# Kernel tuning notes

Measured on AMD Instinct MI355X. Metric: run time of the kernel, lower is better.

The kernel has to match this reference:

```python
import jax, jax.numpy as jnp
import numpy as np

NUM_HEADS = 16
EPS = 1e-5


def setup_inputs() -> dict:
    key = jax.random.key(0)
    ks = jax.random.split(key, 9)
    B, S, D = 2, 2048, 1024
    s = 1.0 / np.sqrt(D)
    return {
        "x": jax.random.normal(ks[0], (B, S, D), dtype=jnp.float32),
        "Wq": jax.random.uniform(ks[1], (D, D), jnp.float32, -s, s),
        "bq": jax.random.uniform(ks[2], (D,), jnp.float32, -s, s),
        "Wk": jax.random.uniform(ks[3], (D, D), jnp.float32, -s, s),
        "bk": jax.random.uniform(ks[4], (D,), jnp.float32, -s, s),
        "Wv": jax.random.uniform(ks[5], (D, D), jnp.float32, -s, s),
        "bv": jax.random.uniform(ks[6], (D,), jnp.float32, -s, s),
        "Wo": jax.random.uniform(ks[7], (D, D), jnp.float32, -s, s),
        "bo": jax.random.uniform(ks[8], (D,), jnp.float32, -s, s),
    }


def reference(x, Wq, bq, Wk, bk, Wv, bv, Wo, bo):
    B, S, D = x.shape
    H = NUM_HEADS
    hd = D // H
    # projections -> [B, H, S, hd]
    def proj(W, b):
        return (x @ W + b).reshape(B, S, H, hd).transpose(0, 2, 1, 3)
    Q = proj(Wq, bq)
    K = proj(Wk, bk)
    V = proj(Wv, bv)
    scores = jnp.einsum("bhqd,bhkd->bhqk", Q, K) / jnp.sqrt(jnp.float32(hd))
    attn = jax.nn.softmax(scores, axis=-1)  # dropout is identity in eval mode
    out = jnp.einsum("bhqk,bhkd->bhqd", attn, V)
    out = out.transpose(0, 2, 1, 3).reshape(B, S, D)
    out = jax.nn.relu(out @ Wo + bo)
    mu = jnp.mean(out, axis=-1, keepdims=True)
    var = jnp.var(out, axis=-1, keepdims=True)
    return (out - mu) * jax.lax.rsqrt(var + EPS)
```

## Files before the change

kernel.cpp:

```cpp
#include <hip/hip_runtime.h>
#include <hip/hip_bf16.h>
#include <math.h>

#define Bb 2
#define Ss 2048
#define Dd 1024
#define Hh 16
#define HD 64
#define Mm (Bb*Ss)

typedef __attribute__((ext_vector_type(8))) short bf8_t;
typedef __attribute__((ext_vector_type(4))) float f4_t;
typedef __attribute__((ext_vector_type(4))) unsigned u4_t;
typedef __attribute__((ext_vector_type(2))) unsigned uint2v;

#define LOG2E 1.4426950408889634f

#define AS1 __attribute__((address_space(1)))
#define AS3 __attribute__((address_space(3)))

__device__ __forceinline__ void gl2lds16(const void* g, void* l) {
    __builtin_amdgcn_global_load_lds((const AS1 unsigned int*)g,
                                     (AS3 unsigned int*)l, 16, 0, 0);
}
__device__ __forceinline__ short bfr(float f) {
    __hip_bfloat16 h = __float2bfloat16(f);
    return *reinterpret_cast<short*>(&h);
}
__device__ __forceinline__ unsigned pkbf16(float a, float b) {
    const unsigned ua = __builtin_bit_cast(unsigned, a) + 0x8000u;
    const unsigned ub = __builtin_bit_cast(unsigned, b) + 0x8000u;
    return __builtin_amdgcn_perm(ub, ua, 0x07060302u);
}
__device__ __forceinline__ float fexp2(float x) {
    return __builtin_amdgcn_exp2f(x);
}
__device__ __forceinline__ float b2f(unsigned short u) {
    return __builtin_bit_cast(float, (unsigned)u << 16);
}
__device__ __forceinline__ void pl32(unsigned &a, unsigned &b) {
#if __has_builtin(__builtin_amdgcn_permlane32_swap)
    uint2v r = __builtin_amdgcn_permlane32_swap(a, b, false, false);
    a = r[0]; b = r[1];
#else
    asm volatile("v_permlane32_swap_b32 %0, %1" : "+v"(a), "+v"(b));
#endif
}
__device__ __forceinline__ void pl16(unsigned &a, unsigned &b) {
#if __has_builtin(__builtin_amdgcn_permlane16_swap)
    uint2v r = __builtin_amdgcn_permlane16_swap(a, b, false, false);
    a = r[0]; b = r[1];
#else
    asm volatile("v_permlane16_swap_b32 %0, %1" : "+v"(a), "+v"(b));
#endif
}

__global__ __launch_bounds__(256)
void prep(const float* __restrict__ x,
          const float* __restrict__ w0, const float* __restrict__ w1,
          const float* __restrict__ w2, const float* __restrict__ w3,
          __hip_bfloat16* __restrict__ Wt4, __hip_bfloat16* __restrict__ Xh)
{
    const int z = blockIdx.z;
    if (z < 4) {
        const float* W = (z == 0) ? w0 : (z == 1) ? w1 : (z == 2) ? w2 : w3;
        __hip_bfloat16* Wt = Wt4 + (size_t)z * Dd * Dd;
        __shared__ float t[32][33];
        const int n0 = blockIdx.x * 32, k0 = blockIdx.y * 32;
        const int tx = threadIdx.x & 31, ty = threadIdx.x >> 5;
        #pragma unroll
        for (int rr = 0; rr < 4; ++rr)
            t[ty + rr*8][tx] = W[(size_t)(k0 + ty + rr*8) * Dd + n0 + tx];
        __syncthreads();
        #pragma unroll
        for (int rr = 0; rr < 4; ++rr)
            Wt[(size_t)(n0 + ty + rr*8) * Dd + k0 + tx] =
                __float2bfloat16(t[tx][ty + rr*8]);
    } else {
        const int bid = (z - 4) * 1024 + blockIdx.y * 32 + blockIdx.x;
        const size_t i = ((size_t)bid * 256 + threadIdx.x) * 8;
        const float4 a = *(const float4*)&x[i];
        const float4 b = *(const float4*)&x[i + 4];
        bf8_t o;
        o[0] = bfr(a.x); o[1] = bfr(a.y); o[2] = bfr(a.z); o[3] = bfr(a.w);
        o[4] = bfr(b.x); o[5] = bfr(b.y); o[6] = bfr(b.z); o[7] = bfr(b.w);
        *(bf8_t*)&Xh[i] = o;
    }
}

__global__ __launch_bounds__(256)
void gemm_qkv(const __hip_bfloat16* __restrict__ A,
              const __hip_bfloat16* __restrict__ Bt,
              const float* __restrict__ b0, const float* __restrict__ b1,
              const float* __restrict__ b2,
              __hip_bfloat16* __restrict__ Qh, __hip_bfloat16* __restrict__ Kh,
              __hip_bfloat16* __restrict__ Vt)
{
    __shared__ __align__(16) char pool[34816];
    __hip_bfloat16* As = (__hip_bfloat16*)pool;
    __hip_bfloat16* Bs = As + 2 * 128 * 32;

    const int lin  = blockIdx.y * 24 + blockIdx.x;
    const int nlin = (lin & 7) * 96 + (lin >> 3);
    const int bx   = nlin % 24;
    const int by   = nlin / 24;

    const int tid  = threadIdx.x;
    const int wave = tid >> 6;
    const int lane = tid & 63;
    const int llo  = lane & 15;
    const int lhi  = lane >> 4;
    const int wm   = wave & 1;
    const int wn   = wave >> 1;
    const int row0 = by * 128;
    const int col0 = bx * 128;

    size_t aoff[2], boff[2];
    int    loff[2];
    #pragma unroll
    for (int p = 0; p < 2; ++p) {
        const int g = p * 256 + wave * 64 + lane;
        const int r = g >> 2;
        const int kc = ((g & 3) ^ ((r >> 1) & 3)) * 8;
        aoff[p] = (size_t)(row0 + r) * Dd + kc;
        boff[p] = (size_t)(col0 + r) * Dd + kc;
        loff[p] = (p * 256 + wave * 64) * 16;
    }
    const __hip_bfloat16* Acur = A;
    const __hip_bfloat16* Bcur = Bt;

    auto stage = [&](int buf) {
        #pragma unroll
        for (int p = 0; p < 2; ++p) {
            gl2lds16(Acur + aoff[p], (char*)As + buf*8192 + loff[p]);
            gl2lds16(Bcur + boff[p], (char*)Bs + buf*8192 + loff[p]);
        }
        Acur += 32; Bcur += 32;
    };

    const int xch = (lhi ^ ((llo >> 1) & 3)) * 8;

    f4_t acc[4][4] = {};
    stage(0);
    for (int kt = 0; kt < 32; ++kt) {
        const int buf = kt & 1;
        __syncthreads();
        if (kt + 1 < 32) stage(buf ^ 1);

        bf8_t a[4], b[4];
        #pragma unroll
        for (int i = 0; i < 4; ++i)
            a[i] = *(const bf8_t*)&As[buf*4096 + (wm*64 + i*16 + llo) * 32 + xch];
        #pragma unroll
        for (int j = 0; j < 4; ++j)
            b[j] = *(const bf8_t*)&Bs[buf*4096 + (wn*64 + j*16 + llo) * 32 + xch];
        #pragma unroll
        for (int i = 0; i < 4; ++i)
            #pragma unroll
            for (int j = 0; j < 4; ++j)
                acc[i][j] = __builtin_amdgcn_mfma_f32_16x16x32_bf16(
                    a[i], b[j], acc[i][j], 0, 0, 0);
    }

    const int sel   = col0 >> 10;
    const int cbase = col0 & 1023;
    __hip_bfloat16* Ls = (__hip_bfloat16*)pool;
    __syncthreads();

    float bv[4];
    const float* bp = (sel == 0) ? b0 : (sel == 1) ? b1 : b2;
    #pragma unroll
    for (int j = 0; j < 4; ++j) bv[j] = bp[cbase + wn*64 + j*16 + llo];
    const float scale = (sel == 0) ? 0.125f * LOG2E : 1.0f;

    if (sel < 2) {
        #pragma unroll
        for (int i = 0; i < 4; ++i)
            #pragma unroll
            for (int r = 0; r < 4; ++r) {
                const int ml = wm*64 + i*16 + lhi*4 + r;
                #pragma unroll
                for (int j = 0; j < 4; ++j)
                    Ls[ml*136 + wn*64 + j*16 + llo] =
                        __float2bfloat16((acc[i][j][r] + bv[j]) * scale);
            }
        __syncthreads();
        __hip_bfloat16* outQK = (sel == 0) ? Qh : Kh;
        #pragma unroll
        for (int p = 0; p < 8; ++p) {
            const int id = p*256 + tid;
            const int rl = id >> 4;
            const int c8 = (id & 15) * 8;
            const bf8_t v = *(const bf8_t*)&Ls[rl*136 + c8];
            const int m  = row0 + rl;
            const int b_ = m >> 11, s_ = m & (Ss - 1);
            const int col = cbase + c8;
            *(bf8_t*)&outQK[((size_t)(b_*Hh + (col >> 6))*Ss + s_)*HD + (col & 63)] = v;
        }
    } else {
        #pragma unroll
        for (int i = 0; i < 4; ++i)
            #pragma unroll
            for (int r = 0; r < 4; ++r) {
                const int ml = wm*64 + i*16 + lhi*4 + r;
                #pragma unroll
                for (int j = 0; j < 4; ++j)
                    Ls[(wn*64 + j*16 + llo)*136 + ml] =
                        __float2bfloat16(acc[i][j][r] + bv[j]);
            }
        __syncthreads();
        const int b_ = row0 >> 11;
        const int sb = row0 & (Ss - 1);
        #pragma unroll
        for (int p = 0; p < 8; ++p) {
            const int cl = p*16 + (tid >> 4);
            const int m  = (tid & 15) * 8;
            const bf8_t v = *(const bf8_t*)&Ls[cl*136 + m];
            const int cc = cbase + cl;
            *(bf8_t*)&Vt[((size_t)(b_*Hh + (cc >> 6))*HD + (cc & 63))*Ss + sb + m] = v;
        }
    }
}

__global__ __launch_bounds__(256, 2)
void attn_mfma(const __hip_bfloat16* __restrict__ Qh,
               const __hip_bfloat16* __restrict__ Kh,
               const __hip_bfloat16* __restrict__ Vt,
               __hip_bfloat16* __restrict__ Ah)
{
    const int lin  = (blockIdx.z * Hh + blockIdx.y) * (Ss/128) + blockIdx.x;
    const int xcd  = lin & 7;
    const int slot = lin >> 3;
    const int grp  = (xcd << 2) | (slot >> 4);
    const int qc   = slot & 15;
    const int b    = grp >> 4;
    const int h    = grp & 15;

    const int wave = threadIdx.x >> 6;
    const int lane = threadIdx.x & 63;
    const int llo  = lane & 15;
    const int lhi  = lane >> 4;
    const int qb   = qc * 128 + wave * 32;

    const size_t base = ((size_t)(b*Hh + h)) * Ss * HD;

    __shared__ __hip_bfloat16 Ks[2][2 * 64 * 32];
    __shared__ __hip_bfloat16 Vs[2][2 * 64 * 32];

    int koff[2], voff[2], loff[2];
    #pragma unroll
    for (int it = 0; it < 2; ++it) {
        const int g  = it*256 + wave*64 + lane;
        const int hf = g >> 8;
        const int rr = (g >> 2) & 63;
        const int c8 = ((g & 3) ^ ((rr >> 1) & 3)) * 8;
        koff[it] = rr*HD + hf*32 + c8;
        voff[it] = rr*Ss + hf*32 + c8;
        loff[it] = (it*256 + wave*64) * 16;
    }
    const __hip_bfloat16* Kcur = Kh + base;
    const __hip_bfloat16* Vcur = Vt + base;

    auto stage = [&](int buf) {
        #pragma unroll
        for (int it = 0; it < 2; ++it) {
            gl2lds16(Kcur + koff[it], (char*)&Ks[buf][0] + loff[it]);
            gl2lds16(Vcur + voff[it], (char*)&Vs[buf][0] + loff[it]);
        }
        Kcur += 64 * HD;
        Vcur += 64;
    };

    bf8_t qf[2][2];
    #pragma unroll
    for (int s = 0; s < 2; ++s)
        #pragma unroll
        for (int d = 0; d < 2; ++d)
            qf[s][d] = *(const bf8_t*)&Qh[base + (size_t)(qb + 16*s + llo)*HD + 32*d + lhi*8];

    f4_t o_[2][4];
    f4_t lsum[2];
    #pragma unroll
    for (int s = 0; s < 2; ++s) {
        #pragma unroll
        for (int n = 0; n < 4; ++n) o_[s][n] = (f4_t){0.f,0.f,0.f,0.f};
        lsum[s] = (f4_t){0.f,0.f,0.f,0.f};
    }
    const short oneb = 0x3F80;
    const bf8_t vones = {oneb,oneb,oneb,oneb,oneb,oneb,oneb,oneb};

    const f4_t zf = {0.f,0.f,0.f,0.f};
    const int xch = (lhi ^ ((llo >> 1) & 3)) * 8;

    bf8_t pfp[2][2];
    bf8_t vfp[4][2];

    stage(0);

    for (int t = 0; t < Ss/64; ++t) {
        const int buf = t & 1;
        __syncthreads();
        if (t + 1 < Ss/64) stage(buf ^ 1);

        bf8_t kf[4][2];
        #pragma unroll
        for (int kc = 0; kc < 4; ++kc)
            #pragma unroll
            for (int d = 0; d < 2; ++d)
                kf[kc][d] = *(const bf8_t*)&Ks[buf][d*2048 + (kc*16 + llo)*32 + xch];

        f4_t sacc[2][4];
        #pragma unroll
        for (int s = 0; s < 2; ++s)
            #pragma unroll
            for (int kc = 0; kc < 4; ++kc) {
                sacc[s][kc] = __builtin_amdgcn_mfma_f32_16x16x32_bf16(kf[kc][0], qf[s][0], zf, 0, 0, 0);
                sacc[s][kc] = __builtin_amdgcn_mfma_f32_16x16x32_bf16(kf[kc][1], qf[s][1], sacc[s][kc], 0, 0, 0);
            }

        if (t > 0) {
            __builtin_amdgcn_s_setprio(1);
            #pragma unroll
            for (int d = 0; d < 2; ++d)
                #pragma unroll
                for (int nc = 0; nc < 4; ++nc)
                    #pragma unroll
                    for (int s = 0; s < 2; ++s)
                        o_[s][nc] = __builtin_amdgcn_mfma_f32_16x16x32_bf16(pfp[s][d], vfp[nc][d], o_[s][nc], 0, 0, 0);
            #pragma unroll
            for (int s = 0; s < 2; ++s)
                #pragma unroll
                for (int d = 0; d < 2; ++d)
                    lsum[s] = __builtin_amdgcn_mfma_f32_16x16x32_bf16(pfp[s][d], vones, lsum[s], 0, 0, 0);
            __builtin_amdgcn_s_setprio(0);
        }

        #pragma unroll
        for (int nc = 0; nc < 4; ++nc)
            #pragma unroll
            for (int d = 0; d < 2; ++d)
                vfp[nc][d] = *(const bf8_t*)&Vs[buf][d*2048 + (nc*16 + llo)*32 + xch];

        #pragma unroll
        for (int s = 0; s < 2; ++s) {
            unsigned w[4][2];
            #pragma unroll
            for (int kc = 0; kc < 4; ++kc) {
                const float p0 = fexp2(sacc[s][kc][0]);
                const float p1 = fexp2(sacc[s][kc][1]);
                const float p2 = fexp2(sacc[s][kc][2]);
                const float p3 = fexp2(sacc[s][kc][3]);
                w[kc][0] = pkbf16(p0, p1);
                w[kc][1] = pkbf16(p2, p3);
            }
            #pragma unroll
            for (int d = 0; d < 2; ++d) {
                u4_t pu;
                #pragma unroll
                for (int hh = 0; hh < 2; ++hh) {
                    unsigned U = w[2*d][hh], V = w[2*d+1][hh];
                    pl32(U, V);
                    pl16(U, V);
                    pu[hh]     = U;
                    pu[2 + hh] = V;
                }
                pfp[s][d] = __builtin_bit_cast(bf8_t, pu);
            }
        }
    }

    #pragma unroll
    for (int d = 0; d < 2; ++d)
        #pragma unroll
        for (int nc = 0; nc < 4; ++nc)
            #pragma unroll
            for (int s = 0; s < 2; ++s)
                o_[s][nc] = __builtin_amdgcn_mfma_f32_16x16x32_bf16(pfp[s][d], vfp[nc][d], o_[s][nc], 0, 0, 0);
    #pragma unroll
    for (int s = 0; s < 2; ++s)
        #pragma unroll
        for (int d = 0; d < 2; ++d)
            lsum[s] = __builtin_amdgcn_mfma_f32_16x16x32_bf16(pfp[s][d], vones, lsum[s], 0, 0, 0);

    #pragma unroll
    for (int s = 0; s < 2; ++s) {
        #pragma unroll
        for (int r = 0; r < 4; ++r) {
            const float inv = 1.0f / lsum[s][r];
            const int q = qb + 16*s + 4*lhi + r;
            __hip_bfloat16* orow = &Ah[((size_t)(b*Ss) + q)*Dd + h*HD + llo];
            #pragma unroll
            for (int nc = 0; nc < 4; ++nc)
                orow[16*nc] = __float2bfloat16(o_[s][nc][r] * inv);
        }
    }
}

__global__ __launch_bounds__(256)
void gemm_out(const __hip_bfloat16* __restrict__ A,
              const __hip_bfloat16* __restrict__ Bt,
              __hip_bfloat16* __restrict__ Ro)
{
    __shared__ __hip_bfloat16 As[2][128 * 32];
    __shared__ __hip_bfloat16 Bs[2][128 * 32];

    const int lin  = (blockIdx.z * 32 + blockIdx.y) * 8 + blockIdx.x;
    const int nlin = (lin & 7) * 64 + (lin >> 3);
    const int bx   = nlin & 7;
    const int rest = nlin >> 3;
    const int by   = rest & 31;
    const int z    = rest >> 5;

    const int tid  = threadIdx.x;
    const int wave = tid >> 6;
    const int lane = tid & 63;
    const int llo  = lane & 15;
    const int lhi  = lane >> 4;
    const int wm   = wave & 1;
    const int wn   = wave >> 1;
    const int row0 = by * 128;
    const int col0 = bx * 128;

    size_t aoff[2], boff[2];
    int    loff[2];
    #pragma unroll
    for (int p = 0; p < 2; ++p) {
        const int g = p * 256 + wave * 64 + lane;
        const int r = g >> 2;
        const int kc = ((g & 3) ^ ((r >> 1) & 3)) * 8;
        aoff[p] = (size_t)(row0 + r) * Dd + kc;
        boff[p] = (size_t)(col0 + r) * Dd + kc;
        loff[p] = (p * 256 + wave * 64) * 16;
    }
    const __hip_bfloat16* Acur = A  + (size_t)z * (Dd/2);
    const __hip_bfloat16* Bcur = Bt + (size_t)z * (Dd/2);

    auto stage = [&](int buf) {
        #pragma unroll
        for (int p = 0; p < 2; ++p) {
            gl2lds16(Acur + aoff[p], (char*)&As[buf][0] + loff[p]);
            gl2lds16(Bcur + boff[p], (char*)&Bs[buf][0] + loff[p]);
        }
        Acur += 32; Bcur += 32;
    };

    const int xch = (lhi ^ ((llo >> 1) & 3)) * 8;

    f4_t acc[4][4] = {};
    stage(0);
    for (int kt = 0; kt < 16; ++kt) {
        const int buf = kt & 1;
        __syncthreads();
        if (kt + 1 < 16) stage(buf ^ 1);

        bf8_t a[4], b[4];
        #pragma unroll
        for (int i = 0; i < 4; ++i)
            a[i] = *(const bf8_t*)&As[buf][(wm*64 + i*16 + llo) * 32 + xch];
        #pragma unroll
        for (int j = 0; j < 4; ++j)
            b[j] = *(const bf8_t*)&Bs[buf][(wn*64 + j*16 + llo) * 32 + xch];
        #pragma unroll
        for (int i = 0; i < 4; ++i)
            #pragma unroll
            for (int j = 0; j < 4; ++j)
                acc[i][j] = __builtin_amdgcn_mfma_f32_16x16x32_bf16(
                    a[i], b[j], acc[i][j], 0, 0, 0);
    }

    __hip_bfloat16* Roz = Ro + (size_t)z * Mm * Dd;
    #pragma unroll
    for (int i = 0; i < 4; ++i) {
        #pragma unroll
        for (int r = 0; r < 4; ++r) {
            const int m = row0 + wm*64 + i*16 + lhi*4 + r;
            #pragma unroll
            for (int j = 0; j < 4; ++j) {
                const int col = col0 + wn*64 + j*16 + llo;
                Roz[(size_t)m * Dd + col] = __float2bfloat16(acc[i][j][r]);
            }
        }
    }
}

__global__ __launch_bounds__(256)
void layernorm(const __hip_bfloat16* __restrict__ P0,
               const __hip_bfloat16* __restrict__ P1,
               const float* __restrict__ bias, float* __restrict__ out)
{
    const int row = blockIdx.x;
    const int c = threadIdx.x;
    const ushort4 a = ((const ushort4*)(P0 + (size_t)row*Dd))[c];
    const ushort4 b = ((const ushort4*)(P1 + (size_t)row*Dd))[c];
    const float4 bb = ((const float4*)bias)[c];
    float4 v;
    v.x = fmaxf(b2f(a.x) + b2f(b.x) + bb.x, 0.0f);
    v.y = fmaxf(b2f(a.y) + b2f(b.y) + bb.y, 0.0f);
    v.z = fmaxf(b2f(a.z) + b2f(b.z) + bb.z, 0.0f);
    v.w = fmaxf(b2f(a.w) + b2f(b.w) + bb.w, 0.0f);

    float s  = v.x + v.y + v.z + v.w;
    float ss = v.x*v.x + v.y*v.y + v.z*v.z + v.w*v.w;
    #pragma unroll
    for (int off = 32; off > 0; off >>= 1) {
        s  += __shfl_down(s,  off);
        ss += __shfl_down(ss, off);
    }
    __shared__ float rs[4], rss[4];
    const int wid = c >> 6, lid = c & 63;
    if (lid == 0) { rs[wid] = s; rss[wid] = ss; }
    __syncthreads();
    s  = rs[0] + rs[1] + rs[2] + rs[3];
    ss = rss[0] + rss[1] + rss[2] + rss[3];
    const float mean = s * (1.0f / Dd);
    const float var  = ss * (1.0f / Dd) - mean * mean;
    const float rstd = rsqrtf(var + 1e-5f);
    float4 o;
    o.x = (v.x - mean) * rstd;
    o.y = (v.y - mean) * rstd;
    o.z = (v.z - mean) * rstd;
    o.w = (v.w - mean) * rstd;
    ((float4*)(out + (size_t)row*Dd))[c] = o;
}

extern "C" void kernel_launch(void* const* d_in, const int* in_sizes, int n_in,
                              void* d_out, int out_size, void* d_ws, size_t ws_size,
                              hipStream_t stream)
{
    const float* x  = (const float*)d_in[0];
    const float* Wq = (const float*)d_in[1];
    const float* bq = (const float*)d_in[2];
    const float* Wk = (const float*)d_in[3];
    const float* bk = (const float*)d_in[4];
    const float* Wv = (const float*)d_in[5];
    const float* bv = (const float*)d_in[6];
    const float* Wo = (const float*)d_in[7];
    const float* bo = (const float*)d_in[8];
    float* out = (float*)d_out;

    __hip_bfloat16* Xh    = (__hip_bfloat16*)d_ws;
    __hip_bfloat16* Wqkvt = Xh    + (size_t)Mm*Dd;
    __hip_bfloat16* Wot   = Wqkvt + (size_t)3*Dd*Dd;
    __hip_bfloat16* Ah    = Wot   + (size_t)Dd*Dd;
    __hip_bfloat16* Qh    = Ah    + (size_t)Mm*Dd;
    __hip_bfloat16* Kh    = Qh    + (size_t)Mm*Dd;
    __hip_bfloat16* Vt    = Kh    + (size_t)Mm*Dd;
    __hip_bfloat16* Rb    = Qh;

    prep<<<dim3(32, 32, 6), dim3(256), 0, stream>>>(x, Wq, Wk, Wv, Wo, Wqkvt, Xh);
    gemm_qkv<<<dim3(3*Dd/128, Mm/128), dim3(256), 0, stream>>>(
        Xh, Wqkvt, bq, bk, bv, Qh, Kh, Vt);
    attn_mfma<<<dim3(Ss/128, Hh, Bb), dim3(256), 0, stream>>>(Qh, Kh, Vt, Ah);
    gemm_out<<<dim3(Dd/128, Mm/128, 2), dim3(256), 0, stream>>>(Ah, Wot, Rb);
    layernorm<<<dim3(Mm), dim3(256), 0, stream>>>(Rb, Rb + (size_t)Mm*Dd, bo, out);
}
```

Measured before the change: 191.2 us.

## Split attention over two key halves and merge partials in a combine kernel

The attention kernel now splits the key/value sequence into two halves, so the grid has twice as many blocks, each looping over half the key tiles. Each half writes unnormalized bf16 outputs and its row sums to separate buffers. A new combine kernel adds the partials and divides by the summed denominators. The launch bound is raised to 4 blocks per CU. This is meant to fix under-filled CUs and low occupancy, at the cost of an extra kernel launch, extra global traffic for the partials, and bf16 rounding of unnormalized values; the merge is only exact if both halves use the same exponent reference.

```diff
diff --git a/kernel.cpp b/kernel.cpp
--- a/kernel.cpp
+++ b/kernel.cpp
@@ -222,17 +222,19 @@
     }
 }
 
-__global__ __launch_bounds__(256, 2)
+__global__ __launch_bounds__(256, 4)
 void attn_mfma(const __hip_bfloat16* __restrict__ Qh,
                const __hip_bfloat16* __restrict__ Kh,
                const __hip_bfloat16* __restrict__ Vt,
-               __hip_bfloat16* __restrict__ Ah)
+               __hip_bfloat16* __restrict__ O0, __hip_bfloat16* __restrict__ O1,
+               float* __restrict__ L0, float* __restrict__ L1)
 {
     const int lin  = (blockIdx.z * Hh + blockIdx.y) * (Ss/128) + blockIdx.x;
     const int xcd  = lin & 7;
     const int slot = lin >> 3;
-    const int grp  = (xcd << 2) | (slot >> 4);
+    const int grp  = (xcd << 2) | (slot >> 5);
     const int qc   = slot & 15;
+    const int sk   = (slot >> 4) & 1;
     const int b    = grp >> 4;
     const int h    = grp & 15;
 
@@ -258,8 +260,8 @@
         voff[it] = rr*Ss + hf*32 + c8;
         loff[it] = (it*256 + wave*64) * 16;
     }
-    const __hip_bfloat16* Kcur = Kh + base;
-    const __hip_bfloat16* Vcur = Vt + base;
+    const __hip_bfloat16* Kcur = Kh + base + (size_t)sk * (Ss/2) * HD;
+    const __hip_bfloat16* Vcur = Vt + base + (size_t)sk * (Ss/2);
 
     auto stage = [&](int buf) {
         #pragma unroll
@@ -297,10 +299,11 @@
 
     stage(0);
 
-    for (int t = 0; t < Ss/64; ++t) {
+    const int NT = Ss/2/64;
+    for (int t = 0; t < NT; ++t) {
         const int buf = t & 1;
         __syncthreads();
-        if (t + 1 < Ss/64) stage(buf ^ 1);
+        if (t + 1 < NT) stage(buf ^ 1);
 
         bf8_t kf[4][2];
         #pragma unroll
@@ -382,18 +385,43 @@
         for (int d = 0; d < 2; ++d)
             lsum[s] = __builtin_amdgcn_mfma_f32_16x16x32_bf16(pfp[s][d], vones, lsum[s], 0, 0, 0);
 
+    __hip_bfloat16* Od = sk ? O1 : O0;
+    float*          Ld = sk ? L1 : L0;
     #pragma unroll
     for (int s = 0; s < 2; ++s) {
         #pragma unroll
         for (int r = 0; r < 4; ++r) {
-            const float inv = 1.0f / lsum[s][r];
             const int q = qb + 16*s + 4*lhi + r;
-            __hip_bfloat16* orow = &Ah[((size_t)(b*Ss) + q)*Dd + h*HD + llo];
+            __hip_bfloat16* orow = &Od[((size_t)(b*Ss) + q)*Dd + h*HD + llo];
             #pragma unroll
             for (int nc = 0; nc < 4; ++nc)
-                orow[16*nc] = __float2bfloat16(o_[s][nc][r] * inv);
-        }
-    }
+                orow[16*nc] = __float2bfloat16(o_[s][nc][r]);
+            if (llo == 0)
+                Ld[((b*Hh + h) << 11) + q] = lsum[s][r];
+        }
+    }
+}
+
+__global__ __launch_bounds__(256)
+void combine(const __hip_bfloat16* __restrict__ O0,
+             const __hip_bfloat16* __restrict__ O1,
+             const float* __restrict__ L0, const float* __restrict__ L1,
+             __hip_bfloat16* __restrict__ Ah)
+{
+    const int gid = blockIdx.x * 256 + threadIdx.x;
+    const int row = gid >> 7;
+    const int c8  = (gid & 127) * 8;
+    const int b_  = row >> 11, s_ = row & (Ss - 1);
+    const int hh  = c8 >> 6;
+    const int li  = ((b_*Hh + hh) << 11) + s_;
+    const float inv = 1.0f / (L0[li] + L1[li]);
+    const bf8_t a = *(const bf8_t*)&O0[(size_t)row*Dd + c8];
+    const bf8_t c = *(const bf8_t*)&O1[(size_t)row*Dd + c8];
+    bf8_t o;
+    #pragma unroll
+    for (int j = 0; j < 8; ++j)
+        o[j] = bfr((b2f((unsigned short)a[j]) + b2f((unsigned short)c[j])) * inv);
+    *(bf8_t*)&Ah[(size_t)row*Dd + c8] = o;
 }
 
 __global__ __launch_bounds__(256)
@@ -545,12 +573,16 @@
     __hip_bfloat16* Qh    = Ah    + (size_t)Mm*Dd;
     __hip_bfloat16* Kh    = Qh    + (size_t)Mm*Dd;
     __hip_bfloat16* Vt    = Kh    + (size_t)Mm*Dd;
+    float*          Lp0   = (float*)(Vt + (size_t)Mm*Dd);
+    float*          Lp1   = Lp0 + (size_t)Bb*Hh*Ss;
     __hip_bfloat16* Rb    = Qh;
 
     prep<<<dim3(32, 32, 6), dim3(256), 0, stream>>>(x, Wq, Wk, Wv, Wo, Wqkvt, Xh);
     gemm_qkv<<<dim3(3*Dd/128, Mm/128), dim3(256), 0, stream>>>(
         Xh, Wqkvt, bq, bk, bv, Qh, Kh, Vt);
-    attn_mfma<<<dim3(Ss/128, Hh, Bb), dim3(256), 0, stream>>>(Qh, Kh, Vt, Ah);
+    attn_mfma<<<dim3(Ss/128, Hh, 2*Bb), dim3(256), 0, stream>>>(
+        Qh, Kh, Vt, Ah, Xh, Lp0, Lp1);
+    combine<<<dim3(Mm*Dd/8/256), dim3(256), 0, stream>>>(Ah, Xh, Lp0, Lp1, Ah);
     gemm_out<<<dim3(Dd/128, Mm/128, 2), dim3(256), 0, stream>>>(Ah, Wot, Rb);
     layernorm<<<dim3(Mm), dim3(256), 0, stream>>>(Rb, Rb + (size_t)Mm*Dd, bo, out);
 }
```

Result: slower. 352.9 us (+84.5%).
